# Optimization experiments

Measured on AMD Instinct MI355X. Metric: run time of the kernel, lower is better.

Reference implementation:

```python
import jax, jax.numpy as jnp
import numpy as np

THRESH = 0.7  # TWN-style threshold factor: delta = 0.7 * mean|W|


def ternarize(W):
    """Quantize latent float weights to alpha * {-1, 0, +1} (per-tensor scale)."""
    absW = jnp.abs(W)
    delta = THRESH * jnp.mean(absW)
    mask = (absW > delta).astype(W.dtype)
    n = jnp.maximum(jnp.sum(mask), 1.0)
    alpha = jnp.sum(absW * mask) / n
    return alpha * jnp.sign(W) * mask


def setup_inputs() -> dict:
    key = jax.random.key(0)
    k_x, k_w1, k_b1, k_w2, k_b2 = jax.random.split(key, 5)
    B = 65536
    x = jax.random.normal(k_x, (B, 784), dtype=jnp.float32)
    # latent float weights (torch Linear layout: [out, in]), kaiming-ish scale
    W1 = jax.random.normal(k_w1, (64, 784), dtype=jnp.float32) * (1.0 / np.sqrt(784))
    b1 = jax.random.normal(k_b1, (64,), dtype=jnp.float32) * 0.01
    W2 = jax.random.normal(k_w2, (10, 64), dtype=jnp.float32) * (1.0 / np.sqrt(64))
    b2 = jax.random.normal(k_b2, (10,), dtype=jnp.float32) * 0.01
    return {"x": x, "W1": W1, "b1": b1, "W2": W2, "b2": b2}


def reference(x, W1, b1, W2, b2):
    x = x.reshape(-1, 784)
    Wq1 = ternarize(W1)  # [64, 784]
    Wq2 = ternarize(W2)  # [10, 64]
    h = jax.nn.relu(x @ Wq1.T + b1)   # [B, 64]
    out = h @ Wq2.T + b2              # [B, 10]
    return out
```

## Files before the change

kernel.cpp:

```cpp
#include <hip/hip_runtime.h>
#include <hip/hip_bf16.h>


typedef __attribute__((ext_vector_type(4))) float f32x4;
typedef __attribute__((ext_vector_type(8))) short s16x8;
typedef __attribute__((ext_vector_type(4))) short s16x4;

#define K1 784
#define K1_PAD 800
#define NHID 64
#define NOUT 10

static __device__ __forceinline__ unsigned short f2bf_rne(float f) {
    unsigned int u = __builtin_bit_cast(unsigned int, f);
    unsigned int r = u + 0x7FFFu + ((u >> 16) & 1u);
    return (unsigned short)(r >> 16);
}

static __device__ double block_sum256(double v, double* red) {
    #pragma unroll
    for (int off = 32; off > 0; off >>= 1) v += __shfl_down(v, off, 64);
    const int w = threadIdx.x >> 6;
    const int lane = threadIdx.x & 63;
    __syncthreads();
    if (lane == 0) red[w] = v;
    __syncthreads();
    return red[0] + red[1] + red[2] + red[3];
}

__global__ __launch_bounds__(256) void tern_sum_kernel(
    const float* __restrict__ W1, const float* __restrict__ W2,
    double* __restrict__ hdr)
{
    __shared__ double red[4];
    double s = 0.0;
    for (int i = blockIdx.x * 256 + threadIdx.x; i < NHID * K1; i += gridDim.x * 256)
        s += (double)fabsf(W1[i]);
    s = block_sum256(s, red);
    if (threadIdx.x == 0) atomicAdd(&hdr[0], s);

    if (blockIdx.x == 0) {
        double s2 = 0.0;
        for (int i = threadIdx.x; i < NOUT * NHID; i += 256)
            s2 += (double)fabsf(W2[i]);
        s2 = block_sum256(s2, red);
        if (threadIdx.x == 0) atomicAdd(&hdr[1], s2);
    }
}

__global__ __launch_bounds__(256) void tern_quant_kernel(
    const float* __restrict__ W1, const float* __restrict__ W2,
    unsigned short* __restrict__ W1q, unsigned short* __restrict__ W2q,
    double* __restrict__ hdr)
{
    __shared__ double red[4];
    const float delta1 = (float)(0.7 * hdr[0] / (double)(NHID * K1));

    double sm = 0.0, cn = 0.0;
    for (int i = blockIdx.x * 256 + threadIdx.x; i < NHID * K1_PAD; i += gridDim.x * 256) {
        int n = i / K1_PAD;
        int k = i - n * K1_PAD;
        unsigned short v = 0;
        if (k < K1) {
            float w = W1[n * K1 + k];
            float a = fabsf(w);
            if (a > delta1) { v = (w > 0.0f) ? 0x3F80u : 0xBF80u; sm += (double)a; cn += 1.0; }
        }
        W1q[i] = v;
    }
    sm = block_sum256(sm, red);
    cn = block_sum256(cn, red);
    if (threadIdx.x == 0) { atomicAdd(&hdr[2], sm); atomicAdd(&hdr[3], cn); }

    if (blockIdx.x == 0) {
        const float delta2 = (float)(0.7 * hdr[1] / (double)(NOUT * NHID));
        double sm2 = 0.0, cn2 = 0.0;
        for (int i = threadIdx.x; i < 16 * NHID; i += 256) {
            int n = i >> 6;
            int k = i & 63;
            unsigned short v = 0;
            if (n < NOUT) {
                float w = W2[n * NHID + k];
                float a = fabsf(w);
                if (a > delta2) { v = (w > 0.0f) ? 0x3F80u : 0xBF80u; sm2 += (double)a; cn2 += 1.0; }
            }
            W2q[i] = v;
        }
        sm2 = block_sum256(sm2, red);
        cn2 = block_sum256(cn2, red);
        if (threadIdx.x == 0) { atomicAdd(&hdr[4], sm2); atomicAdd(&hdr[5], cn2); }
    }
}

__global__ __launch_bounds__(256) void fused_kernel(
    const float* __restrict__ x,
    const float* __restrict__ b1,
    const float* __restrict__ b2,
    const short* __restrict__ W1q,
    const short* __restrict__ W2q,
    const double* __restrict__ hdr,
    float* __restrict__ out)
{
    const int tid  = threadIdx.x;
    const int wave = tid >> 6;
    const int lane = tid & 63;
    const int low  = lane & 15;
    const int quad = lane >> 4;

    const int m0 = blockIdx.x * 64 + wave * 16;

    const int srow = lane >> 3;
    const int scol = lane & 7;
    const float* g0 = x + (size_t)(m0 + srow) * K1 + scol * 4;
    const float* g1 = x + (size_t)(m0 + 8 + srow) * K1 + scol * 4;

    __shared__ __align__(16) unsigned short stage[4][2][16][32];
    __shared__ __align__(16) unsigned short h_lds[4][16][72];

    const short* wbase = W1q + (size_t)low * K1_PAD + quad * 8;

    f32x4 acc[4];
    #pragma unroll
    for (int nt = 0; nt < 4; ++nt) acc[nt] = (f32x4){0.f, 0.f, 0.f, 0.f};

    const f32x4 zero4 = (f32x4){0.f, 0.f, 0.f, 0.f};

    f32x4 c0 = *(const f32x4*)(g0);
    f32x4 c1 = *(const f32x4*)(g1);

    int buf = 0;
    for (int ks = 0; ks < 25; ++ks) {
        f32x4 n0 = zero4, n1 = zero4;
        if (ks < 24) {
            const int kf = (ks + 1) * 32 + scol * 4;
            if (kf < K1) {
                n0 = *(const f32x4*)(g0 + (ks + 1) * 32);
                n1 = *(const f32x4*)(g1 + (ks + 1) * 32);
            }
        }

        s16x4 p0, p1;
        p0[0] = (short)f2bf_rne(c0[0]); p0[1] = (short)f2bf_rne(c0[1]);
        p0[2] = (short)f2bf_rne(c0[2]); p0[3] = (short)f2bf_rne(c0[3]);
        p1[0] = (short)f2bf_rne(c1[0]); p1[1] = (short)f2bf_rne(c1[1]);
        p1[2] = (short)f2bf_rne(c1[2]); p1[3] = (short)f2bf_rne(c1[3]);
        *(s16x4*)&stage[wave][buf][srow][scol * 4]     = p0;
        *(s16x4*)&stage[wave][buf][8 + srow][scol * 4] = p1;

        __asm__ volatile("s_waitcnt lgkmcnt(0)" ::: "memory");

        s16x8 a = *(const s16x8*)&stage[wave][buf][low][quad * 8];
        const short* wk = wbase + ks * 32;
        #pragma unroll
        for (int nt = 0; nt < 4; ++nt) {
            s16x8 b = *(const s16x8*)(wk + (size_t)nt * 16 * K1_PAD);
            acc[nt] = __builtin_amdgcn_mfma_f32_16x16x32_bf16(a, b, acc[nt], 0, 0, 0);
        }

        c0 = n0; c1 = n1; buf ^= 1;
    }

    const float alpha1 = (float)(hdr[2] / fmax(hdr[3], 1.0));
    const float alpha2 = (float)(hdr[4] / fmax(hdr[5], 1.0));

    #pragma unroll
    for (int nt = 0; nt < 4; ++nt) {
        const int n = nt * 16 + low;
        const float bias = b1[n];
        #pragma unroll
        for (int r = 0; r < 4; ++r) {
            float hv = fmaxf(0.0f, fmaf(alpha1, acc[nt][r], bias));
            h_lds[wave][quad * 4 + r][n] = f2bf_rne(hv);
        }
    }
    __asm__ volatile("s_waitcnt lgkmcnt(0)" ::: "memory");

    s16x8 a0 = *(const s16x8*)(&h_lds[wave][low][quad * 8]);
    s16x8 a1 = *(const s16x8*)(&h_lds[wave][low][32 + quad * 8]);
    s16x8 w0 = *(const s16x8*)(W2q + low * 64 + quad * 8);
    s16x8 w1 = *(const s16x8*)(W2q + low * 64 + 32 + quad * 8);

    f32x4 acc2 = (f32x4){0.f, 0.f, 0.f, 0.f};
    acc2 = __builtin_amdgcn_mfma_f32_16x16x32_bf16(a0, w0, acc2, 0, 0, 0);
    acc2 = __builtin_amdgcn_mfma_f32_16x16x32_bf16(a1, w1, acc2, 0, 0, 0);

    if (low < NOUT) {
        const float bias2 = b2[low];
        #pragma unroll
        for (int r = 0; r < 4; ++r) {
            const int row = m0 + quad * 4 + r;
            out[(size_t)row * NOUT + low] = fmaf(alpha2, acc2[r], bias2);
        }
    }
}

extern "C" void kernel_launch(void* const* d_in, const int* in_sizes, int n_in,
                              void* d_out, int out_size, void* d_ws, size_t ws_size,
                              hipStream_t stream) {
    const float* x  = (const float*)d_in[0];
    const float* W1 = (const float*)d_in[1];
    const float* b1 = (const float*)d_in[2];
    const float* W2 = (const float*)d_in[3];
    const float* b2 = (const float*)d_in[4];
    float* out = (float*)d_out;

    const int nrows = in_sizes[0] / K1;

    double* hdr = (double*)d_ws;
    unsigned short* W1q = (unsigned short*)((char*)d_ws + 64);
    unsigned short* W2q = W1q + NHID * K1_PAD;

    hipMemsetAsync(d_ws, 0, 64, stream);

    tern_sum_kernel<<<64, 256, 0, stream>>>(W1, W2, hdr);
    tern_quant_kernel<<<64, 256, 0, stream>>>(W1, W2, W1q, W2q, hdr);

    const int nblocks = nrows / 64;
    fused_kernel<<<nblocks, 256, 0, stream>>>(x, b1, b2, (const short*)W1q,
                                              (const short*)W2q, hdr, out);
}
```

Baseline: 307.6 us.

## Merge ternarization into one single-block kernel and use packed bf16 convert

Replaces the memset plus two multi-block ternarization kernels with one 1024-thread single-block kernel. It computes the mean, threshold, quantized weights and alpha scales in place and writes the final alphas directly, with no atomics. It also swaps the scalar software bf16 rounding in the main GEMM loop for the packed v_cvt_pk_bf16_f32 instruction. This removes two launches and the atomics, but the weight prep now runs serially on one CU, which may cost more than the launches it saves.

Result: slower. 344.8 us (+12.1%).

```diff
diff --git a/kernel.cpp b/kernel.cpp
--- a/kernel.cpp
+++ b/kernel.cpp
@@ -5,6 +5,7 @@
 typedef __attribute__((ext_vector_type(4))) float f32x4;
 typedef __attribute__((ext_vector_type(8))) short s16x8;
 typedef __attribute__((ext_vector_type(4))) short s16x4;
+typedef __attribute__((ext_vector_type(2))) unsigned int u32x2;
 
 #define K1 784
 #define K1_PAD 800
@@ -17,7 +18,13 @@
     return (unsigned short)(r >> 16);
 }
 
-static __device__ double block_sum256(double v, double* red) {
+static __device__ __forceinline__ unsigned int cvt_pk_bf16(float lo, float hi) {
+    unsigned int r;
+    asm("v_cvt_pk_bf16_f32 %0, %1, %2" : "=v"(r) : "v"(lo), "v"(hi));
+    return r;
+}
+
+static __device__ double block_sum1024(double v, double* red) {
     #pragma unroll
     for (int off = 32; off > 0; off >>= 1) v += __shfl_down(v, off, 64);
     const int w = threadIdx.x >> 6;
@@ -25,70 +32,65 @@
     __syncthreads();
     if (lane == 0) red[w] = v;
     __syncthreads();
-    return red[0] + red[1] + red[2] + red[3];
-}
-
-__global__ __launch_bounds__(256) void tern_sum_kernel(
-    const float* __restrict__ W1, const float* __restrict__ W2,
-    double* __restrict__ hdr)
-{
-    __shared__ double red[4];
     double s = 0.0;
-    for (int i = blockIdx.x * 256 + threadIdx.x; i < NHID * K1; i += gridDim.x * 256)
-        s += (double)fabsf(W1[i]);
-    s = block_sum256(s, red);
-    if (threadIdx.x == 0) atomicAdd(&hdr[0], s);
-
-    if (blockIdx.x == 0) {
-        double s2 = 0.0;
-        for (int i = threadIdx.x; i < NOUT * NHID; i += 256)
-            s2 += (double)fabsf(W2[i]);
-        s2 = block_sum256(s2, red);
-        if (threadIdx.x == 0) atomicAdd(&hdr[1], s2);
-    }
-}
-
-__global__ __launch_bounds__(256) void tern_quant_kernel(
+    #pragma unroll
+    for (int i = 0; i < 16; ++i) s += red[i];
+    return s;
+}
+
+__global__ __launch_bounds__(1024) void tern_all_kernel(
     const float* __restrict__ W1, const float* __restrict__ W2,
     unsigned short* __restrict__ W1q, unsigned short* __restrict__ W2q,
     double* __restrict__ hdr)
 {
-    __shared__ double red[4];
-    const float delta1 = (float)(0.7 * hdr[0] / (double)(NHID * K1));
-
-    double sm = 0.0, cn = 0.0;
-    for (int i = blockIdx.x * 256 + threadIdx.x; i < NHID * K1_PAD; i += gridDim.x * 256) {
+    __shared__ double red[16];
+    const int tid = threadIdx.x;
+
+    double s1 = 0.0;
+    for (int i = tid; i < NHID * K1; i += 1024)
+        s1 += (double)fabsf(W1[i]);
+    double s2 = 0.0;
+    for (int i = tid; i < NOUT * NHID; i += 1024)
+        s2 += (double)fabsf(W2[i]);
+    s1 = block_sum1024(s1, red);
+    s2 = block_sum1024(s2, red);
+
+    const float delta1 = (float)(0.7 * s1 / (double)(NHID * K1));
+    const float delta2 = (float)(0.7 * s2 / (double)(NOUT * NHID));
+
+    double sm1 = 0.0, cn1 = 0.0;
+    for (int i = tid; i < NHID * K1_PAD; i += 1024) {
         int n = i / K1_PAD;
         int k = i - n * K1_PAD;
         unsigned short v = 0;
         if (k < K1) {
             float w = W1[n * K1 + k];
             float a = fabsf(w);
-            if (a > delta1) { v = (w > 0.0f) ? 0x3F80u : 0xBF80u; sm += (double)a; cn += 1.0; }
+            if (a > delta1) { v = (w > 0.0f) ? 0x3F80u : 0xBF80u; sm1 += (double)a; cn1 += 1.0; }
         }
         W1q[i] = v;
     }
-    sm = block_sum256(sm, red);
-    cn = block_sum256(cn, red);
-    if (threadIdx.x == 0) { atomicAdd(&hdr[2], sm); atomicAdd(&hdr[3], cn); }
-
-    if (blockIdx.x == 0) {
-        const float delta2 = (float)(0.7 * hdr[1] / (double)(NOUT * NHID));
-        double sm2 = 0.0, cn2 = 0.0;
-        for (int i = threadIdx.x; i < 16 * NHID; i += 256) {
-            int n = i >> 6;
-            int k = i & 63;
-            unsigned short v = 0;
-            if (n < NOUT) {
-                float w = W2[n * NHID + k];
-                float a = fabsf(w);
-                if (a > delta2) { v = (w > 0.0f) ? 0x3F80u : 0xBF80u; sm2 += (double)a; cn2 += 1.0; }
-            }
-            W2q[i] = v;
-        }
-        sm2 = block_sum256(sm2, red);
-        cn2 = block_sum256(cn2, red);
-        if (threadIdx.x == 0) { atomicAdd(&hdr[4], sm2); atomicAdd(&hdr[5], cn2); }
+
+    double sm2 = 0.0, cn2 = 0.0;
+    for (int i = tid; i < 16 * NHID; i += 1024) {
+        int n = i >> 6;
+        int k = i & 63;
+        unsigned short v = 0;
+        if (n < NOUT) {
+            float w = W2[n * NHID + k];
+            float a = fabsf(w);
+            if (a > delta2) { v = (w > 0.0f) ? 0x3F80u : 0xBF80u; sm2 += (double)a; cn2 += 1.0; }
+        }
+        W2q[i] = v;
+    }
+
+    sm1 = block_sum1024(sm1, red);
+    cn1 = block_sum1024(cn1, red);
+    sm2 = block_sum1024(sm2, red);
+    cn2 = block_sum1024(cn2, red);
+    if (tid == 0) {
+        hdr[0] = sm1 / fmax(cn1, 1.0);
+        hdr[1] = sm2 / fmax(cn2, 1.0);
     }
 }
 
@@ -139,13 +141,13 @@
             }
         }
 
-        s16x4 p0, p1;
-        p0[0] = (short)f2bf_rne(c0[0]); p0[1] = (short)f2bf_rne(c0[1]);
-        p0[2] = (short)f2bf_rne(c0[2]); p0[3] = (short)f2bf_rne(c0[3]);
-        p1[0] = (short)f2bf_rne(c1[0]); p1[1] = (short)f2bf_rne(c1[1]);
-        p1[2] = (short)f2bf_rne(c1[2]); p1[3] = (short)f2bf_rne(c1[3]);
-        *(s16x4*)&stage[wave][buf][srow][scol * 4]     = p0;
-        *(s16x4*)&stage[wave][buf][8 + srow][scol * 4] = p1;
+        u32x2 p0, p1;
+        p0[0] = cvt_pk_bf16(c0[0], c0[1]);
+        p0[1] = cvt_pk_bf16(c0[2], c0[3]);
+        p1[0] = cvt_pk_bf16(c1[0], c1[1]);
+        p1[1] = cvt_pk_bf16(c1[2], c1[3]);
+        *(u32x2*)&stage[wave][buf][srow][scol * 4]     = p0;
+        *(u32x2*)&stage[wave][buf][8 + srow][scol * 4] = p1;
 
         __asm__ volatile("s_waitcnt lgkmcnt(0)" ::: "memory");
 
@@ -160,8 +162,8 @@
         c0 = n0; c1 = n1; buf ^= 1;
     }
 
-    const float alpha1 = (float)(hdr[2] / fmax(hdr[3], 1.0));
-    const float alpha2 = (float)(hdr[4] / fmax(hdr[5], 1.0));
+    const float alpha1 = (float)hdr[0];
+    const float alpha2 = (float)hdr[1];
 
     #pragma unroll
     for (int nt = 0; nt < 4; ++nt) {
@@ -210,10 +212,7 @@
     unsigned short* W1q = (unsigned short*)((char*)d_ws + 64);
     unsigned short* W2q = W1q + NHID * K1_PAD;
 
-    hipMemsetAsync(d_ws, 0, 64, stream);
-
-    tern_sum_kernel<<<64, 256, 0, stream>>>(W1, W2, hdr);
-    tern_quant_kernel<<<64, 256, 0, stream>>>(W1, W2, W1q, W2q, hdr);
+    tern_all_kernel<<<1, 1024, 0, stream>>>(W1, W2, W1q, W2q, hdr);
 
     const int nblocks = nrows / 64;
     fused_kernel<<<nblocks, 256, 0, stream>>>(x, b1, b2, (const short*)W1q,
```

## Drop memset and atomics, prefetch weight fragments, use packed bf16 convert

Applied to the files above, without the earlier changes.

Replaces the atomic accumulation and memset with per-block partial sums written to workspace, reduced by later kernels (tern_quant sums 64 partials, the fused kernel reduces psm/pcn with wave shuffles). In the main GEMM loop, the W1q B-fragments for the next k-step are prefetched into registers alongside the x loads. The manual fp32→bf16 rounding is replaced with the v_cvt_pk_bf16_f32 instruction. This removes a memset launch and atomic traffic and hides weight-load latency, at the cost of extra registers and a small per-wave reduction.

Measured after the change: 312.2 us. Within noise of the previous version (+1.5%).

```diff
diff --git a/kernel.cpp b/kernel.cpp
--- a/kernel.cpp
+++ b/kernel.cpp
@@ -4,7 +4,7 @@
 
 typedef __attribute__((ext_vector_type(4))) float f32x4;
 typedef __attribute__((ext_vector_type(8))) short s16x8;
-typedef __attribute__((ext_vector_type(4))) short s16x4;
+typedef __attribute__((ext_vector_type(2))) unsigned int u32x2;
 
 #define K1 784
 #define K1_PAD 800
@@ -15,6 +15,12 @@
     unsigned int u = __builtin_bit_cast(unsigned int, f);
     unsigned int r = u + 0x7FFFu + ((u >> 16) & 1u);
     return (unsigned short)(r >> 16);
+}
+
+static __device__ __forceinline__ unsigned int cvt_pk_bf16(float lo, float hi) {
+    unsigned int r;
+    asm("v_cvt_pk_bf16_f32 %0, %1, %2" : "=v"(r) : "v"(lo), "v"(hi));
+    return r;
 }
 
 static __device__ double block_sum256(double v, double* red) {
@@ -28,67 +34,80 @@
     return red[0] + red[1] + red[2] + red[3];
 }
 
+
 __global__ __launch_bounds__(256) void tern_sum_kernel(
     const float* __restrict__ W1, const float* __restrict__ W2,
-    double* __restrict__ hdr)
+    double* __restrict__ p1, double* __restrict__ p2)
 {
     __shared__ double red[4];
+    const int gid = blockIdx.x * 256 + threadIdx.x;
+
     double s = 0.0;
-    for (int i = blockIdx.x * 256 + threadIdx.x; i < NHID * K1; i += gridDim.x * 256)
-        s += (double)fabsf(W1[i]);
+    if (gid < (NHID * K1) / 4) {
+        f32x4 v = ((const f32x4*)W1)[gid];
+        s = (double)fabsf(v[0]) + (double)fabsf(v[1])
+          + (double)fabsf(v[2]) + (double)fabsf(v[3]);
+    }
     s = block_sum256(s, red);
-    if (threadIdx.x == 0) atomicAdd(&hdr[0], s);
+    if (threadIdx.x == 0) p1[blockIdx.x] = s;
 
     if (blockIdx.x == 0) {
         double s2 = 0.0;
-        for (int i = threadIdx.x; i < NOUT * NHID; i += 256)
-            s2 += (double)fabsf(W2[i]);
+        if (threadIdx.x < (NOUT * NHID) / 4) {
+            f32x4 v = ((const f32x4*)W2)[threadIdx.x];
+            s2 = (double)fabsf(v[0]) + (double)fabsf(v[1])
+               + (double)fabsf(v[2]) + (double)fabsf(v[3]);
+        }
         s2 = block_sum256(s2, red);
-        if (threadIdx.x == 0) atomicAdd(&hdr[1], s2);
+        if (threadIdx.x == 0) p2[0] = s2;
     }
 }
 
 __global__ __launch_bounds__(256) void tern_quant_kernel(
     const float* __restrict__ W1, const float* __restrict__ W2,
     unsigned short* __restrict__ W1q, unsigned short* __restrict__ W2q,
-    double* __restrict__ hdr)
+    const double* __restrict__ p1, const double* __restrict__ p2,
+    double* __restrict__ psm, double* __restrict__ pcn,
+    double* __restrict__ a2)
 {
     __shared__ double red[4];
-    const float delta1 = (float)(0.7 * hdr[0] / (double)(NHID * K1));
-
+
+    double v = (threadIdx.x < 64) ? p1[threadIdx.x] : 0.0;
+    const double s1 = block_sum256(v, red);
+    const float delta1 = (float)(0.7 * s1 / (double)(NHID * K1));
+
+    const int n = blockIdx.x;
     double sm = 0.0, cn = 0.0;
-    for (int i = blockIdx.x * 256 + threadIdx.x; i < NHID * K1_PAD; i += gridDim.x * 256) {
-        int n = i / K1_PAD;
-        int k = i - n * K1_PAD;
-        unsigned short v = 0;
+    for (int k = threadIdx.x; k < K1_PAD; k += 256) {
+        unsigned short q = 0;
         if (k < K1) {
             float w = W1[n * K1 + k];
             float a = fabsf(w);
-            if (a > delta1) { v = (w > 0.0f) ? 0x3F80u : 0xBF80u; sm += (double)a; cn += 1.0; }
-        }
-        W1q[i] = v;
+            if (a > delta1) { q = (w > 0.0f) ? 0x3F80u : 0xBF80u; sm += (double)a; cn += 1.0; }
+        }
+        W1q[n * K1_PAD + k] = q;
     }
     sm = block_sum256(sm, red);
     cn = block_sum256(cn, red);
-    if (threadIdx.x == 0) { atomicAdd(&hdr[2], sm); atomicAdd(&hdr[3], cn); }
+    if (threadIdx.x == 0) { psm[n] = sm; pcn[n] = cn; }
 
     if (blockIdx.x == 0) {
-        const float delta2 = (float)(0.7 * hdr[1] / (double)(NOUT * NHID));
+        const float delta2 = (float)(0.7 * p2[0] / (double)(NOUT * NHID));
         double sm2 = 0.0, cn2 = 0.0;
         for (int i = threadIdx.x; i < 16 * NHID; i += 256) {
-            int n = i >> 6;
+            int r = i >> 6;
             int k = i & 63;
-            unsigned short v = 0;
-            if (n < NOUT) {
-                float w = W2[n * NHID + k];
+            unsigned short q = 0;
+            if (r < NOUT) {
+                float w = W2[r * NHID + k];
                 float a = fabsf(w);
-                if (a > delta2) { v = (w > 0.0f) ? 0x3F80u : 0xBF80u; sm2 += (double)a; cn2 += 1.0; }
+                if (a > delta2) { q = (w > 0.0f) ? 0x3F80u : 0xBF80u; sm2 += (double)a; cn2 += 1.0; }
             }
-            W2q[i] = v;
+            W2q[i] = q;
         }
         sm2 = block_sum256(sm2, red);
         cn2 = block_sum256(cn2, red);
-        if (threadIdx.x == 0) { atomicAdd(&hdr[4], sm2); atomicAdd(&hdr[5], cn2); }
+        if (threadIdx.x == 0) a2[0] = sm2 / fmax(cn2, 1.0);
     }
 }
 
@@ -98,7 +117,9 @@
     const float* __restrict__ b2,
     const short* __restrict__ W1q,
     const short* __restrict__ W2q,
-    const double* __restrict__ hdr,
+    const double* __restrict__ psm,
+    const double* __restrict__ pcn,
+    const double* __restrict__ a2,
     float* __restrict__ out)
 {
     const int tid  = threadIdx.x;
@@ -127,11 +148,20 @@
 
     f32x4 c0 = *(const f32x4*)(g0);
     f32x4 c1 = *(const f32x4*)(g1);
+    s16x8 bf[4];
+    #pragma unroll
+    for (int nt = 0; nt < 4; ++nt)
+        bf[nt] = *(const s16x8*)(wbase + (size_t)nt * 16 * K1_PAD);
 
     int buf = 0;
     for (int ks = 0; ks < 25; ++ks) {
         f32x4 n0 = zero4, n1 = zero4;
+        s16x8 bn[4];
         if (ks < 24) {
+            const short* wn = wbase + (ks + 1) * 32;
+            #pragma unroll
+            for (int nt = 0; nt < 4; ++nt)
+                bn[nt] = *(const s16x8*)(wn + (size_t)nt * 16 * K1_PAD);
             const int kf = (ks + 1) * 32 + scol * 4;
             if (kf < K1) {
                 n0 = *(const f32x4*)(g0 + (ks + 1) * 32);
@@ -139,29 +169,36 @@
             }
         }
 
-        s16x4 p0, p1;
-        p0[0] = (short)f2bf_rne(c0[0]); p0[1] = (short)f2bf_rne(c0[1]);
-        p0[2] = (short)f2bf_rne(c0[2]); p0[3] = (short)f2bf_rne(c0[3]);
-        p1[0] = (short)f2bf_rne(c1[0]); p1[1] = (short)f2bf_rne(c1[1]);
-        p1[2] = (short)f2bf_rne(c1[2]); p1[3] = (short)f2bf_rne(c1[3]);
-        *(s16x4*)&stage[wave][buf][srow][scol * 4]     = p0;
-        *(s16x4*)&stage[wave][buf][8 + srow][scol * 4] = p1;
+        u32x2 p0, p1;
+        p0[0] = cvt_pk_bf16(c0[0], c0[1]);
+        p0[1] = cvt_pk_bf16(c0[2], c0[3]);
+        p1[0] = cvt_pk_bf16(c1[0], c1[1]);
+        p1[1] = cvt_pk_bf16(c1[2], c1[3]);
+        *(u32x2*)&stage[wave][buf][srow][scol * 4]     = p0;
+        *(u32x2*)&stage[wave][buf][8 + srow][scol * 4] = p1;
 
         __asm__ volatile("s_waitcnt lgkmcnt(0)" ::: "memory");
 
         s16x8 a = *(const s16x8*)&stage[wave][buf][low][quad * 8];
-        const short* wk = wbase + ks * 32;
-        #pragma unroll
-        for (int nt = 0; nt < 4; ++nt) {
-            s16x8 b = *(const s16x8*)(wk + (size_t)nt * 16 * K1_PAD);
-            acc[nt] = __builtin_amdgcn_mfma_f32_16x16x32_bf16(a, b, acc[nt], 0, 0, 0);
-        }
-
+        #pragma unroll
+        for (int nt = 0; nt < 4; ++nt)
+            acc[nt] = __builtin_amdgcn_mfma_f32_16x16x32_bf16(a, bf[nt], acc[nt], 0, 0, 0);
+
+        #pragma unroll
+        for (int nt = 0; nt < 4; ++nt) bf[nt] = bn[nt];
         c0 = n0; c1 = n1; buf ^= 1;
     }
 
-    const float alpha1 = (float)(hdr[2] / fmax(hdr[3], 1.0));
-    const float alpha2 = (float)(hdr[4] / fmax(hdr[5], 1.0));
+    double vs = psm[lane], vc = pcn[lane];
+    #pragma unroll
+    for (int off = 32; off > 0; off >>= 1) {
+        vs += __shfl_down(vs, off, 64);
+        vc += __shfl_down(vc, off, 64);
+    }
+    vs = __shfl(vs, 0, 64);
+    vc = __shfl(vc, 0, 64);
+    const float alpha1 = (float)(vs / fmax(vc, 1.0));
+    const float alpha2 = (float)a2[0];
 
     #pragma unroll
     for (int nt = 0; nt < 4; ++nt) {
@@ -206,16 +243,19 @@
 
     const int nrows = in_sizes[0] / K1;
 
-    double* hdr = (double*)d_ws;
-    unsigned short* W1q = (unsigned short*)((char*)d_ws + 64);
+    char* base = (char*)d_ws;
+    double* p1  = (double*)(base);
+    double* psm = (double*)(base + 512);
+    double* pcn = (double*)(base + 1024);
+    double* p2  = (double*)(base + 1536);
+    double* a2  = (double*)(base + 1544);
+    unsigned short* W1q = (unsigned short*)(base + 2048);
     unsigned short* W2q = W1q + NHID * K1_PAD;
 
-    hipMemsetAsync(d_ws, 0, 64, stream);
-
-    tern_sum_kernel<<<64, 256, 0, stream>>>(W1, W2, hdr);
-    tern_quant_kernel<<<64, 256, 0, stream>>>(W1, W2, W1q, W2q, hdr);
+    tern_sum_kernel<<<64, 256, 0, stream>>>(W1, W2, p1, p2);
+    tern_quant_kernel<<<64, 256, 0, stream>>>(W1, W2, W1q, W2q, p1, p2, psm, pcn, a2);
 
     const int nblocks = nrows / 64;
     fused_kernel<<<nblocks, 256, 0, stream>>>(x, b1, b2, (const short*)W1q,
-                                              (const short*)W2q, hdr, out);
-}
+                                              (const short*)W2q, psm, pcn, a2, out);
+}
```
